# Optimization experiments

Measured on AMD Instinct MI355X. Metric: run time of the kernel, lower is better.

## Reference

```python
import jax, jax.numpy as jnp
import numpy as np
import math

HIDDEN = 256
D = 256  # attention_head_size (num_heads=1)
LN_EPS = 1e-5


def setup_inputs() -> dict:
    key = jax.random.key(0)
    ks = jax.random.split(key, 12)
    b, n = 8, 256
    s = 0.02
    return {
        "hidden_states": jax.random.normal(ks[0], (b, n, HIDDEN), jnp.float32),
        "structure_matrix": jax.random.normal(ks[1], (b, n, n, D), jnp.float32),
        "Wq": jax.random.normal(ks[2], (HIDDEN, D), jnp.float32) * s,
        "bq": jnp.zeros((D,), jnp.float32),
        "Wk": jax.random.normal(ks[3], (D, D), jnp.float32) * s,
        "bk": jnp.zeros((D,), jnp.float32),
        "Wv": jax.random.normal(ks[4], (HIDDEN, D), jnp.float32) * s,
        "bv": jnp.zeros((D,), jnp.float32),
        "Wo": jax.random.normal(ks[5], (D, D), jnp.float32) * s,
        "bo": jnp.zeros((D,), jnp.float32),
        "ln_gamma": jnp.ones((D,), jnp.float32),
        "ln_beta": jnp.zeros((D,), jnp.float32),
    }


def _layer_norm(x, gamma, beta):
    mu = jnp.mean(x, axis=-1, keepdims=True)
    var = jnp.mean(jnp.square(x - mu), axis=-1, keepdims=True)
    return (x - mu) * jax.lax.rsqrt(var + LN_EPS) * gamma + beta


def reference(hidden_states, structure_matrix, Wq, bq, Wk, bk, Wv, bv, Wo, bo, ln_gamma, ln_beta):
    # projections
    q = hidden_states @ Wq + bq            # [b, n, d]
    k = structure_matrix @ Wk + bk         # [b, l, r, d]
    v = hidden_states @ Wv + bv            # [b, n, d]
    # pair-biased attention: each (l, r) pair attends over all n tokens
    scores = jnp.einsum('bnd,blrd->blrn', q, k) / math.sqrt(D)  # [b, l, r, n]
    probs = jax.nn.softmax(scores, axis=-1)  # dropout is identity in eval
    ctx = jnp.einsum('blrn,bnd->blrd', probs, v)  # [b, l, r, d]
    out = ctx @ Wo + bo
    return _layer_norm(out + structure_matrix, ln_gamma, ln_beta)
```

## Files before the change

### kernel.cpp

```cpp
#include <hip/hip_runtime.h>
#include <hip/hip_bf16.h>

typedef __attribute__((ext_vector_type(8))) short short8v;
typedef __attribute__((ext_vector_type(4))) float f32x4;
typedef __attribute__((ext_vector_type(8))) unsigned short us8;
typedef const __attribute__((address_space(1))) void* gas_t;
typedef __attribute__((address_space(3))) void* las_t;

__device__ __forceinline__ unsigned short f2bf(float f) {
  union { __hip_bfloat16 h; unsigned short u; } c;
  c.h = __float2bfloat16(f);
  return c.u;
}
__device__ __forceinline__ unsigned int f2bf2(float lo, float hi) {
  union { __hip_bfloat162 h; unsigned int u; } c;
  c.h = __float22bfloat162_rn(make_float2(lo, hi));
  return c.u;
}

__global__ __launch_bounds__(256) void make_w(
    const float* __restrict__ Wq, const float* __restrict__ Wk,
    const float* __restrict__ Wv, const float* __restrict__ Wo,
    const float* __restrict__ bq, const float* __restrict__ bk,
    const float* __restrict__ bv, float* __restrict__ WA,
    float* __restrict__ WB, float* __restrict__ wb2,
    float* __restrict__ cq, float* __restrict__ cv, float* __restrict__ cb) {
  __shared__ float wq[256], wv[256], bqs[256], bvs[256];
  const int i = blockIdx.x, t = threadIdx.x;
  wq[t] = Wq[i * 256 + t];
  wv[t] = Wv[i * 256 + t];
  bqs[t] = bq[t];
  bvs[t] = bv[t];
  __syncthreads();
  float sa = 0.f, sb = 0.f;
#pragma unroll 8
  for (int d = 0; d < 256; d++) {
    sa = fmaf(wq[d], Wk[t * 256 + d], sa);
    sb = fmaf(wv[d], Wo[d * 256 + t], sb);
  }
  WA[i * 256 + t] = sa * 0.0625f;
  WB[i * 256 + t] = sb;
  if (t == 0) {
    float s = 0.f;
#pragma unroll 8
    for (int d = 0; d < 256; d++) s = fmaf(wq[d], bk[d], s);
    wb2[i] = s * 0.0625f;
  }
  if (i == 0) {
    float s1 = 0.f, s2 = 0.f;
#pragma unroll 8
    for (int d = 0; d < 256; d++) {
      s1 = fmaf(bqs[d], Wk[t * 256 + d], s1);
      s2 = fmaf(bvs[d], Wo[d * 256 + t], s2);
    }
    cq[t] = s1 * 0.0625f;
    cv[t] = s2;
    if (t == 0) {
      float s = 0.f;
      for (int d = 0; d < 256; d++) s = fmaf(bk[d], bqs[d], s);
      cb[0] = s * 0.0625f;
    }
  }
}

__global__ __launch_bounds__(256) void bn_k(
    const float* __restrict__ hs, const float* __restrict__ wb2,
    const float* __restrict__ cb, float* __restrict__ ebn) {
  __shared__ float w2s[256];
  const int b = blockIdx.x, t = threadIdx.x;
  w2s[t] = wb2[t];
  __syncthreads();
  const float* row = hs + (size_t)(b * 256 + t) * 256;
  float s = cb[0];
#pragma unroll 8
  for (int d = 0; d < 256; d++) s = fmaf(row[d], w2s[d], s);
  ebn[b * 256 + t] = __expf(s);
}

__global__ __launch_bounds__(256) void prep2(
    const float* __restrict__ hs, const float* __restrict__ WA,
    const float* __restrict__ WB, const float* __restrict__ cq,
    const float* __restrict__ cv, const float* __restrict__ ebn,
    unsigned short* __restrict__ W2c, unsigned short* __restrict__ V2c) {
  __shared__ float rows[8][256];
  const int tid = threadIdx.x;
  const int g0 = blockIdx.x * 8;
#pragma unroll
  for (int j = 0; j < 8; j++) rows[j][tid] = hs[(size_t)(g0 + j) * 256 + tid];
  __syncthreads();
  const float cqv = cq[tid], cvv = cv[tid];
  float aq[8], av[8];
#pragma unroll
  for (int j = 0; j < 8; j++) { aq[j] = cqv; av[j] = cvv; }
#pragma unroll 8
  for (int i = 0; i < 256; i++) {
    const float wa = WA[i * 256 + tid];
    const float wb = WB[i * 256 + tid];
#pragma unroll
    for (int j = 0; j < 8; j++) {
      aq[j] = fmaf(rows[j][i], wa, aq[j]);
      av[j] = fmaf(rows[j][i], wb, av[j]);
    }
  }
  const int bb = g0 >> 8, n0 = g0 & 255;
  {
    const int kc = tid >> 5, lh = (tid >> 3) & 3, j8 = tid & 7;
    unsigned short* dst = W2c + bb * 65536 + kc * 8192 + (n0 >> 4) * 512 +
                          lh * 128 + (n0 & 15) * 8 + j8;
#pragma unroll
    for (int jj = 0; jj < 8; jj++) dst[jj * 8] = f2bf(aq[jj]);
  }
  {
    const int kc = n0 >> 5, lh = (n0 >> 3) & 3;
    us8 vp;
#pragma unroll
    for (int j = 0; j < 8; j++)
      vp[j] = f2bf(av[j] * ebn[bb * 256 + n0 + j]);
    *(us8*)(V2c + bb * 65536 + kc * 8192 + (tid >> 4) * 512 + lh * 128 +
            (tid & 15) * 8) = vp;
  }
}

__device__ __forceinline__ void stage_b(const unsigned short* src,
                                        unsigned short* lds, int lane) {
#pragma unroll
  for (int i = 0; i < 4; i++)
    __builtin_amdgcn_global_load_lds((gas_t)(src + i * 512 + lane * 8),
                                     (las_t)(lds + i * 512), 16, 0, 0);
}

__global__ __launch_bounds__(256, 2) void pair_attn13(
    const float* __restrict__ S, const float* __restrict__ bo,
    const float* __restrict__ gamma, const float* __restrict__ beta,
    const float* __restrict__ ebn, const unsigned short* __restrict__ W2c,
    const unsigned short* __restrict__ V2c, float* __restrict__ out) {
  __shared__ unsigned short sB[4][8192];
  __shared__ unsigned short sE[4096];

  const int tid = threadIdx.x;
  const int w = tid >> 6;
  const int lane = tid & 63;
  const int l16 = lane & 15;
  const int lhi = lane >> 4;
  const int bid = blockIdx.x;
  const int idx = (bid & 7) * 1024 + (bid >> 3);
  const int rblk = idx & 3;
  const int lrow = (idx >> 2) & 255;
  const int bat = idx >> 10;

  const size_t base = ((size_t)((bat * 256 + lrow) * 256 + rblk * 64)) * 256;
  const float* Srow = S + base + (size_t)(w * 16 + l16) * 256;

  short8v sf[8];
#pragma unroll
  for (int kc = 0; kc < 8; kc++) {
    const float4 u = *(const float4*)(Srow + kc * 32 + lhi * 8);
    const float4 v = *(const float4*)(Srow + kc * 32 + lhi * 8 + 4);
    us8 p;
    unsigned int* pu = (unsigned int*)&p;
    pu[0] = f2bf2(u.x, u.y);
    pu[1] = f2bf2(u.z, u.w);
    pu[2] = f2bf2(v.x, v.y);
    pu[3] = f2bf2(v.z, v.w);
    sf[kc] = *(short8v*)&p;
  }

  {
    const unsigned short eb = f2bf(ebn[bat * 256 + tid]);
    unsigned short* d0 =
        sE + (tid >> 5) * 512 + ((tid >> 3) & 3) * 128 + (tid & 7);
#pragma unroll
    for (int t = 0; t < 16; t++) d0[t * 8] = eb;
  }

  asm volatile("s_waitcnt lgkmcnt(0)" ::: "memory");
  asm volatile("s_waitcnt vmcnt(0)" ::: "memory");
  __builtin_amdgcn_sched_barrier(0);

  const unsigned short* W2b = W2c + (size_t)bat * 65536;
  const unsigned short* V2b = V2c + (size_t)bat * 65536;

  stage_b(W2b + 0 * 8192 + w * 2048, &sB[0][w * 2048], lane);
  stage_b(W2b + 1 * 8192 + w * 2048, &sB[1][w * 2048], lane);
  stage_b(W2b + 2 * 8192 + w * 2048, &sB[2][w * 2048], lane);

  f32x4 acc[16];
  f32x4 accE = (f32x4){0.f, 0.f, 0.f, 0.f};
  unsigned int pkd[32];
#pragma unroll
  for (int t = 0; t < 16; t++) acc[t] = (f32x4){0.f, 0.f, 0.f, 0.f};

  const int A0 = (l16 + ((lhi & 1) * 32)) * 4;
  const int A1 = A0 + 64;
  const bool lo = (lhi < 2);

#pragma unroll
  for (int t = 0; t < 16; t++) {
    if (t < 14) {
      asm volatile("s_waitcnt vmcnt(8)" ::: "memory");
    } else if (t == 14) {
      asm volatile("s_waitcnt vmcnt(4)" ::: "memory");
    } else {
      asm volatile("s_waitcnt vmcnt(0)" ::: "memory");
    }
    __builtin_amdgcn_s_barrier();
    if (t + 3 < 16) {
      const int t3 = t + 3;
      const unsigned short* src =
          (t3 < 8) ? (W2b + t3 * 8192) : (V2b + (t3 - 8) * 8192);
      stage_b(src + w * 2048, &sB[t3 & 3][w * 2048], lane);
    }
    __builtin_amdgcn_sched_barrier(0);
    const unsigned short* bbuf = &sB[t & 3][0];

    if (t < 8) {
      __builtin_amdgcn_s_setprio(1);
#pragma unroll
      for (int nt = 0; nt < 16; nt++) {
        const short8v af = *(const short8v*)(bbuf + nt * 512 + lane * 8);
        acc[nt] = __builtin_amdgcn_mfma_f32_16x16x32_bf16(af, sf[t], acc[nt],
                                                          0, 0, 0);
      }
      __builtin_amdgcn_s_setprio(0);
      if (t == 7) {
#pragma unroll
        for (int nt = 0; nt < 16; nt++) {
          const float p0 = __expf(acc[nt][0]);
          const float p1 = __expf(acc[nt][1]);
          const float p2 = __expf(acc[nt][2]);
          const float p3 = __expf(acc[nt][3]);
          pkd[nt * 2] = f2bf2(p0, p1);
          pkd[nt * 2 + 1] = f2bf2(p2, p3);
          acc[nt] = (f32x4){0.f, 0.f, 0.f, 0.f};
        }
      }
    } else {
      const int qq = t - 8;
      const unsigned int e0 = __builtin_amdgcn_ds_bpermute(A0, pkd[4 * qq + 0]);
      const unsigned int o0 = __builtin_amdgcn_ds_bpermute(A0, pkd[4 * qq + 2]);
      const unsigned int e1 = __builtin_amdgcn_ds_bpermute(A0, pkd[4 * qq + 1]);
      const unsigned int o1 = __builtin_amdgcn_ds_bpermute(A0, pkd[4 * qq + 3]);
      const unsigned int e2 = __builtin_amdgcn_ds_bpermute(A1, pkd[4 * qq + 0]);
      const unsigned int o2 = __builtin_amdgcn_ds_bpermute(A1, pkd[4 * qq + 2]);
      const unsigned int e3 = __builtin_amdgcn_ds_bpermute(A1, pkd[4 * qq + 1]);
      const unsigned int o3 = __builtin_amdgcn_ds_bpermute(A1, pkd[4 * qq + 3]);
      union { unsigned int u[4]; short8v v; } bp_;
      bp_.u[0] = lo ? e0 : o0;
      bp_.u[1] = lo ? e1 : o1;
      bp_.u[2] = lo ? e2 : o2;
      bp_.u[3] = lo ? e3 : o3;
      const short8v bp = bp_.v;
      const short8v ae = *(const short8v*)(sE + qq * 512 + lane * 8);
      __builtin_amdgcn_s_setprio(1);
      accE = __builtin_amdgcn_mfma_f32_16x16x32_bf16(ae, bp, accE, 0, 0, 0);
#pragma unroll
      for (int ct = 0; ct < 16; ct++) {
        const short8v af = *(const short8v*)(bbuf + ct * 512 + lane * 8);
        acc[ct] =
            __builtin_amdgcn_mfma_f32_16x16x32_bf16(af, bp, acc[ct], 0, 0, 0);
      }
      __builtin_amdgcn_s_setprio(0);
    }
  }
  __builtin_amdgcn_sched_barrier(0);

  const float inv = 1.f / accE[0];
  float s1 = 0.f, s2 = 0.f;
#pragma unroll
  for (int ct = 0; ct < 16; ct++) {
    const float4 rz = *(const float4*)(Srow + ct * 16 + lhi * 4);
    const float4 b4 = *(const float4*)(bo + ct * 16 + lhi * 4);
    f32x4 v;
    v[0] = acc[ct][0] * inv + b4.x + rz.x;
    v[1] = acc[ct][1] * inv + b4.y + rz.y;
    v[2] = acc[ct][2] * inv + b4.z + rz.z;
    v[3] = acc[ct][3] * inv + b4.w + rz.w;
#pragma unroll
    for (int g = 0; g < 4; g++) {
      s1 += v[g];
      s2 = fmaf(v[g], v[g], s2);
    }
    acc[ct] = v;
  }
  s1 += __shfl_xor(s1, 16); s2 += __shfl_xor(s2, 16);
  s1 += __shfl_xor(s1, 32); s2 += __shfl_xor(s2, 32);
  const float mean = s1 * (1.f / 256.f);
  const float rstd = rsqrtf(s2 * (1.f / 256.f) - mean * mean + 1e-5f);
  float* Orow = out + base + (size_t)(w * 16 + l16) * 256;
#pragma unroll
  for (int ct = 0; ct < 16; ct++) {
    const float4 g4 = *(const float4*)(gamma + ct * 16 + lhi * 4);
    const float4 be4 = *(const float4*)(beta + ct * 16 + lhi * 4);
    float4 ov;
    ov.x = (acc[ct][0] - mean) * rstd * g4.x + be4.x;
    ov.y = (acc[ct][1] - mean) * rstd * g4.y + be4.y;
    ov.z = (acc[ct][2] - mean) * rstd * g4.z + be4.z;
    ov.w = (acc[ct][3] - mean) * rstd * g4.w + be4.w;
    *(float4*)(Orow + ct * 16 + lhi * 4) = ov;
  }
}

extern "C" void kernel_launch(void* const* d_in, const int* in_sizes, int n_in,
                              void* d_out, int out_size, void* d_ws, size_t ws_size,
                              hipStream_t stream) {
  const float* hs    = (const float*)d_in[0];
  const float* S     = (const float*)d_in[1];
  const float* Wq    = (const float*)d_in[2];
  const float* bq    = (const float*)d_in[3];
  const float* Wk    = (const float*)d_in[4];
  const float* bk    = (const float*)d_in[5];
  const float* Wv    = (const float*)d_in[6];
  const float* bv    = (const float*)d_in[7];
  const float* Wo    = (const float*)d_in[8];
  const float* bo    = (const float*)d_in[9];
  const float* gamma = (const float*)d_in[10];
  const float* beta  = (const float*)d_in[11];

  unsigned short* W2c = (unsigned short*)d_ws;
  unsigned short* V2c = W2c + 8 * 256 * 256;
  float* WA  = (float*)(V2c + 8 * 256 * 256);
  float* WB  = WA + 256 * 256;
  float* wb2 = WB + 256 * 256;
  float* cq  = wb2 + 256;
  float* cv  = cq + 256;
  float* cb  = cv + 256;
  float* ebn = cb + 256;

  make_w<<<256, 256, 0, stream>>>(Wq, Wk, Wv, Wo, bq, bk, bv, WA, WB, wb2, cq,
                                  cv, cb);
  bn_k<<<8, 256, 0, stream>>>(hs, wb2, cb, ebn);
  prep2<<<256, 256, 0, stream>>>(hs, WA, WB, cq, cv, ebn, W2c, V2c);
  pair_attn13<<<8192, 256, 0, stream>>>(S, bo, gamma, beta, ebn, W2c, V2c,
                                        (float*)d_out);
}
```

Before: 556.8 us.

## Fold token bias into softmax exponent, compute row sum directly, triple-buffer for occupancy 3

The per-token bias term is now added to the scores before exponentiation rather than being folded into V as exp(bias). The softmax denominator comes from a register sum with cross-lane shuffles, which removes the extra MFMA and the sE LDS table. The LDS staging ring drops from four buffers to three, and launch bounds ask for three blocks per CU, trading prefetch depth for occupancy. Denominator precision changes slightly: the sum is now taken in fp32 instead of from bf16 inputs.

```diff
diff --git a/kernel.cpp b/kernel.cpp
--- a/kernel.cpp
+++ b/kernel.cpp
@@ -65,7 +65,7 @@
 
 __global__ __launch_bounds__(256) void bn_k(
     const float* __restrict__ hs, const float* __restrict__ wb2,
-    const float* __restrict__ cb, float* __restrict__ ebn) {
+    const float* __restrict__ cb, float* __restrict__ bn) {
   __shared__ float w2s[256];
   const int b = blockIdx.x, t = threadIdx.x;
   w2s[t] = wb2[t];
@@ -74,14 +74,14 @@
   float s = cb[0];
 #pragma unroll 8
   for (int d = 0; d < 256; d++) s = fmaf(row[d], w2s[d], s);
-  ebn[b * 256 + t] = __expf(s);
+  bn[b * 256 + t] = s;
 }
 
 __global__ __launch_bounds__(256) void prep2(
     const float* __restrict__ hs, const float* __restrict__ WA,
     const float* __restrict__ WB, const float* __restrict__ cq,
-    const float* __restrict__ cv, const float* __restrict__ ebn,
-    unsigned short* __restrict__ W2c, unsigned short* __restrict__ V2c) {
+    const float* __restrict__ cv, unsigned short* __restrict__ W2c,
+    unsigned short* __restrict__ V2c) {
   __shared__ float rows[8][256];
   const int tid = threadIdx.x;
   const int g0 = blockIdx.x * 8;
@@ -114,8 +114,7 @@
     const int kc = n0 >> 5, lh = (n0 >> 3) & 3;
     us8 vp;
 #pragma unroll
-    for (int j = 0; j < 8; j++)
-      vp[j] = f2bf(av[j] * ebn[bb * 256 + n0 + j]);
+    for (int j = 0; j < 8; j++) vp[j] = f2bf(av[j]);
     *(us8*)(V2c + bb * 65536 + kc * 8192 + (tid >> 4) * 512 + lh * 128 +
             (tid & 15) * 8) = vp;
   }
@@ -129,13 +128,13 @@
                                      (las_t)(lds + i * 512), 16, 0, 0);
 }
 
-__global__ __launch_bounds__(256, 2) void pair_attn13(
+__global__ __launch_bounds__(256, 3) void pair_attn14(
     const float* __restrict__ S, const float* __restrict__ bo,
     const float* __restrict__ gamma, const float* __restrict__ beta,
-    const float* __restrict__ ebn, const unsigned short* __restrict__ W2c,
+    const float* __restrict__ bn, const unsigned short* __restrict__ W2c,
     const unsigned short* __restrict__ V2c, float* __restrict__ out) {
-  __shared__ unsigned short sB[4][8192];
-  __shared__ unsigned short sE[4096];
+  __shared__ unsigned short sB[3][8192];
+  __shared__ float sBn[256];
 
   const int tid = threadIdx.x;
   const int w = tid >> 6;
@@ -165,13 +164,7 @@
     sf[kc] = *(short8v*)&p;
   }
 
-  {
-    const unsigned short eb = f2bf(ebn[bat * 256 + tid]);
-    unsigned short* d0 =
-        sE + (tid >> 5) * 512 + ((tid >> 3) & 3) * 128 + (tid & 7);
-#pragma unroll
-    for (int t = 0; t < 16; t++) d0[t * 8] = eb;
-  }
+  sBn[tid] = bn[bat * 256 + tid];
 
   asm volatile("s_waitcnt lgkmcnt(0)" ::: "memory");
   asm volatile("s_waitcnt vmcnt(0)" ::: "memory");
@@ -182,11 +175,10 @@
 
   stage_b(W2b + 0 * 8192 + w * 2048, &sB[0][w * 2048], lane);
   stage_b(W2b + 1 * 8192 + w * 2048, &sB[1][w * 2048], lane);
-  stage_b(W2b + 2 * 8192 + w * 2048, &sB[2][w * 2048], lane);
 
   f32x4 acc[16];
-  f32x4 accE = (f32x4){0.f, 0.f, 0.f, 0.f};
   unsigned int pkd[32];
+  float psum = 0.f;
 #pragma unroll
   for (int t = 0; t < 16; t++) acc[t] = (f32x4){0.f, 0.f, 0.f, 0.f};
 
@@ -196,22 +188,20 @@
 
 #pragma unroll
   for (int t = 0; t < 16; t++) {
-    if (t < 14) {
-      asm volatile("s_waitcnt vmcnt(8)" ::: "memory");
-    } else if (t == 14) {
+    if (t < 15) {
       asm volatile("s_waitcnt vmcnt(4)" ::: "memory");
     } else {
       asm volatile("s_waitcnt vmcnt(0)" ::: "memory");
     }
     __builtin_amdgcn_s_barrier();
-    if (t + 3 < 16) {
-      const int t3 = t + 3;
+    if (t + 2 < 16) {
+      const int t2 = t + 2;
       const unsigned short* src =
-          (t3 < 8) ? (W2b + t3 * 8192) : (V2b + (t3 - 8) * 8192);
-      stage_b(src + w * 2048, &sB[t3 & 3][w * 2048], lane);
+          (t2 < 8) ? (W2b + t2 * 8192) : (V2b + (t2 - 8) * 8192);
+      stage_b(src + w * 2048, &sB[t2 % 3][w * 2048], lane);
     }
     __builtin_amdgcn_sched_barrier(0);
-    const unsigned short* bbuf = &sB[t & 3][0];
+    const unsigned short* bbuf = &sB[t % 3][0];
 
     if (t < 8) {
       __builtin_amdgcn_s_setprio(1);
@@ -225,14 +215,18 @@
       if (t == 7) {
 #pragma unroll
         for (int nt = 0; nt < 16; nt++) {
-          const float p0 = __expf(acc[nt][0]);
-          const float p1 = __expf(acc[nt][1]);
-          const float p2 = __expf(acc[nt][2]);
-          const float p3 = __expf(acc[nt][3]);
+          const f32x4 b4 = *(const f32x4*)(sBn + nt * 16 + lhi * 4);
+          const float p0 = __expf(acc[nt][0] + b4[0]);
+          const float p1 = __expf(acc[nt][1] + b4[1]);
+          const float p2 = __expf(acc[nt][2] + b4[2]);
+          const float p3 = __expf(acc[nt][3] + b4[3]);
+          psum += (p0 + p1) + (p2 + p3);
           pkd[nt * 2] = f2bf2(p0, p1);
           pkd[nt * 2 + 1] = f2bf2(p2, p3);
           acc[nt] = (f32x4){0.f, 0.f, 0.f, 0.f};
         }
+        psum += __shfl_xor(psum, 16);
+        psum += __shfl_xor(psum, 32);
       }
     } else {
       const int qq = t - 8;
@@ -250,9 +244,7 @@
       bp_.u[2] = lo ? e2 : o2;
       bp_.u[3] = lo ? e3 : o3;
       const short8v bp = bp_.v;
-      const short8v ae = *(const short8v*)(sE + qq * 512 + lane * 8);
       __builtin_amdgcn_s_setprio(1);
-      accE = __builtin_amdgcn_mfma_f32_16x16x32_bf16(ae, bp, accE, 0, 0, 0);
 #pragma unroll
       for (int ct = 0; ct < 16; ct++) {
         const short8v af = *(const short8v*)(bbuf + ct * 512 + lane * 8);
@@ -264,7 +256,7 @@
   }
   __builtin_amdgcn_sched_barrier(0);
 
-  const float inv = 1.f / accE[0];
+  const float inv = 1.f / psum;
   float s1 = 0.f, s2 = 0.f;
 #pragma unroll
   for (int ct = 0; ct < 16; ct++) {
@@ -324,12 +316,12 @@
   float* cq  = wb2 + 256;
   float* cv  = cq + 256;
   float* cb  = cv + 256;
-  float* ebn = cb + 256;
+  float* bnp = cb + 256;
 
   make_w<<<256, 256, 0, stream>>>(Wq, Wk, Wv, Wo, bq, bk, bv, WA, WB, wb2, cq,
                                   cv, cb);
-  bn_k<<<8, 256, 0, stream>>>(hs, wb2, cb, ebn);
-  prep2<<<256, 256, 0, stream>>>(hs, WA, WB, cq, cv, ebn, W2c, V2c);
-  pair_attn13<<<8192, 256, 0, stream>>>(S, bo, gamma, beta, ebn, W2c, V2c,
+  bn_k<<<8, 256, 0, stream>>>(hs, wb2, cb, bnp);
+  prep2<<<256, 256, 0, stream>>>(hs, WA, WB, cq, cv, W2c, V2c);
+  pair_attn14<<<8192, 256, 0, stream>>>(S, bo, gamma, beta, bnp, W2c, V2c,
                                         (float*)d_out);
 }
```

Result: faster. 533.3 us (-4.2%).
